# Performance work log

Hardware: AMD Instinct MI355X
Metric: run time of the kernel (lower is better)

The kernel has to match this reference:

```python
import jax, jax.numpy as jnp
import numpy as np
import math

INPUT_SIZE = 512
DK = 64
B, N = 8, 2048

def setup_inputs() -> dict:
    key = jax.random.key(0)
    k1, k2, k3, k4, k5, k6 = jax.random.split(key, 6)
    X = jax.random.normal(k1, (B, N, INPUT_SIZE), dtype=jnp.float32)
    h = jax.random.normal(k2, (B, N, INPUT_SIZE), dtype=jnp.float32)
    s = 1.0 / math.sqrt(INPUT_SIZE)
    WQ = jax.random.uniform(k3, (INPUT_SIZE, DK), dtype=jnp.float32, minval=-s, maxval=s)
    bQ = jax.random.uniform(k4, (DK,), dtype=jnp.float32, minval=-s, maxval=s)
    WK = jax.random.uniform(k5, (INPUT_SIZE, DK), dtype=jnp.float32, minval=-s, maxval=s)
    bK = jax.random.uniform(k6, (DK,), dtype=jnp.float32, minval=-s, maxval=s)
    return {"X": X, "h": h, "WQ": WQ, "bQ": bQ, "WK": WK, "bK": bK}

def reference(X, h, WQ, bQ, WK, bK):
    # Q = linearQ(h), K = linearK(X); dropout is eval-mode identity
    Q = jnp.einsum('bnd,dk->bnk', h, WQ) + bQ   # [B, N, dk]
    K = jnp.einsum('bnd,dk->bnk', X, WK) + bK   # [B, N, dk]
    scores = jnp.einsum('bqk,bnk->bqn', Q, K) / jnp.sqrt(jnp.asarray(DK, X.dtype))
    A = jax.nn.softmax(scores, axis=-1)          # [B, N, N]
    out = jnp.einsum('bqn,bnd->bqd', A, X)       # V = X
    return out
```

## Files before the change

### kernel.cpp

```cpp
#include <hip/hip_runtime.h>
#include <hip/hip_bf16.h>

#define B_ 8
#define N_ 2048
#define D_ 512
#define DK_ 64

typedef float f32x4 __attribute__((ext_vector_type(4)));
typedef short bf16x8 __attribute__((ext_vector_type(8)));
typedef unsigned short u16;

__device__ __forceinline__ u16 f2bf(float f) {
  union { float f; unsigned u; } v; v.f = f;
  unsigned r = v.u + 0x7FFFu + ((v.u >> 16) & 1u);
  return (u16)(r >> 16);
}

#define MFMA32(a, b, cacc) __builtin_amdgcn_mfma_f32_16x16x32_bf16((a), (b), (cacc), 0, 0, 0)

#define BARRIER_LGKM() do {                                   \
    asm volatile("s_waitcnt lgkmcnt(0)" ::: "memory");        \
    __builtin_amdgcn_s_barrier();                             \
    asm volatile("" ::: "memory");                            \
  } while (0)


__global__ __launch_bounds__(256) void prep_kernel(
    const float* __restrict__ h, const float* __restrict__ X,
    const float* __restrict__ WQ, const float* __restrict__ bQ,
    const float* __restrict__ WK, const float* __restrict__ bK,
    u16* __restrict__ Qf, u16* __restrict__ Kf, u16* __restrict__ Vf) {
  int bid = blockIdx.x;
  int b = bid & 7, nt = bid >> 3;
  int n0 = nt * 64;
  int t = threadIdx.x, w = t >> 6, l = t & 63, g = l >> 4, c = l & 15;

  __shared__ u16 Xb16[64][520];

  int arow = n0 + w * 16 + c;
  const float* hrow = h + ((size_t)b * N_ + arow) * D_;
  const float* Xrow = X + ((size_t)b * N_ + arow) * D_;
  f32x4 accq[4], acck[4];
#pragma unroll
  for (int cf = 0; cf < 4; ++cf) {
    accq[cf] = (f32x4){0.f, 0.f, 0.f, 0.f};
    acck[cf] = (f32x4){0.f, 0.f, 0.f, 0.f};
  }
  for (int k0 = 0; k0 < D_; k0 += 32) {
    bf16x8 ah, ax;
    {
      f32x4 h0 = *reinterpret_cast<const f32x4*>(hrow + k0 + 8 * g);
      f32x4 h1 = *reinterpret_cast<const f32x4*>(hrow + k0 + 8 * g + 4);
      f32x4 x0 = *reinterpret_cast<const f32x4*>(Xrow + k0 + 8 * g);
      f32x4 x1 = *reinterpret_cast<const f32x4*>(Xrow + k0 + 8 * g + 4);
#pragma unroll
      for (int i = 0; i < 4; ++i) {
        ah[i] = (short)f2bf(h0[i]); ah[i + 4] = (short)f2bf(h1[i]);
        ax[i] = (short)f2bf(x0[i]); ax[i + 4] = (short)f2bf(x1[i]);
      }
    }
    *reinterpret_cast<bf16x8*>(&Xb16[w * 16 + c][k0 + 8 * g]) = ax;
#pragma unroll
    for (int cf = 0; cf < 4; ++cf) {
      bf16x8 bq, bk;
#pragma unroll
      for (int i = 0; i < 8; ++i) {
        int kk = k0 + 8 * g + i;
        bq[i] = (short)f2bf(WQ[(size_t)kk * DK_ + cf * 16 + c]);
        bk[i] = (short)f2bf(WK[(size_t)kk * DK_ + cf * 16 + c]);
      }
      accq[cf] = MFMA32(ah, bq, accq[cf]);
      acck[cf] = MFMA32(ax, bk, acck[cf]);
    }
  }
#pragma unroll
  for (int cf = 0; cf < 4; ++cf) {
    float vq = bQ[cf * 16 + c], vk = bK[cf * 16 + c];
    int ks = cf >> 1;
    int g2 = ((cf & 1) * 16 + c) >> 3;
    int i2 = c & 7;
#pragma unroll
    for (int r = 0; r < 4; ++r) {
      size_t e = ((size_t)(b * 128 + nt * 4 + w) * 2 + ks) * 512 +
                 (g2 * 16 + 4 * g + r) * 8 + i2;
      Qf[e] = f2bf((accq[cf][r] + vq) * 0.125f);
      Kf[e] = f2bf(acck[cf][r] + vk);
    }
  }

  __syncthreads();

#pragma unroll
  for (int dtl = 0; dtl < 8; ++dtl) {
    int dt = w * 8 + dtl;
#pragma unroll
    for (int ks = 0; ks < 2; ++ks) {
      bf16x8 v;
#pragma unroll
      for (int i = 0; i < 8; ++i) v[i] = Xb16[ks * 32 + 8 * g + i][dt * 16 + c];
      *reinterpret_cast<bf16x8*>(
          Vf + (((size_t)(b * 32 + dt) * 32 + nt) * 2 + ks) * 512 + l * 8) = v;
    }
  }
}

__global__ __launch_bounds__(512, 1) void attn_kernel(
    const u16* __restrict__ Qf, const u16* __restrict__ Kf,
    const u16* __restrict__ Vf, float* __restrict__ out) {
  int bid = blockIdx.x;
  int b = bid & 7, qt = bid >> 3;
  int q0 = qt * 64;
  int t = threadIdx.x, w = t >> 6, l = t & 63, g = l >> 4, c = l & 15;
  int qh = w >> 1, kq = w & 1;

  __shared__ u16 Plds[4][64][40];
  __shared__ float Lp[2][64];

  bf16x8 aq[2];
#pragma unroll
  for (int ks = 0; ks < 2; ++ks)
    aq[ks] = *reinterpret_cast<const bf16x8*>(
        Qf + ((size_t)(b * 128 + qt * 4 + qh) * 2 + ks) * 512 + l * 8);

  f32x4 o[4][4];
#pragma unroll
  for (int a = 0; a < 4; ++a)
#pragma unroll
    for (int d = 0; d < 4; ++d) o[a][d] = (f32x4){0.f, 0.f, 0.f, 0.f};
  float lp[4] = {0.f, 0.f, 0.f, 0.f};

  const u16* Kbase = Kf + ((size_t)(b * 256 + 2 * kq)) * 512 + l * 8;
  const u16* Vbase = Vf + ((size_t)(b * 32 + w * 4) * 64) * 512 + l * 8;

  bf16x8 kbuf[4][2], vbuf[4][4];

#pragma unroll
  for (int j = 0; j < 4; ++j) {
#pragma unroll
    for (int ks = 0; ks < 2; ++ks)
      kbuf[j][ks] = *reinterpret_cast<const bf16x8*>(
          Kbase + (size_t)(4 * j + ks) * 512);
#pragma unroll
    for (int f = 0; f < 4; ++f)
      vbuf[j][f] = *reinterpret_cast<const bf16x8*>(
          Vbase + (size_t)(f * 64 + j) * 512);
  }
#pragma unroll
  for (int j0 = 0; j0 < 2; ++j0) {
    f32x4 s = (f32x4){0.f, 0.f, 0.f, 0.f};
    s = MFMA32(aq[0], kbuf[j0][0], s);
    s = MFMA32(aq[1], kbuf[j0][1], s);
#pragma unroll
    for (int r = 0; r < 4; ++r) {
      float p = __expf(s[r]); lp[r] += p;
      Plds[j0][qh * 16 + 4 * g + r][kq * 16 + c] = f2bf(p);
    }
  }
  BARRIER_LGKM();

  auto pair = [&](bf16x8 (&kS0)[2], bf16x8 (&kS1)[2],
                  bf16x8 (&kL0)[2], bf16x8 (&kL1)[2],
                  bf16x8 (&vR0)[4], bf16x8 (&vR1)[4],
                  int k2, int pW0, int pW1, int pR0, int pR1) {
    const int jA = (k2 + 4) & 63, jB = (k2 + 5) & 63;

#pragma unroll
    for (int ks = 0; ks < 2; ++ks)
      kL0[ks] = *reinterpret_cast<const bf16x8*>(
          Kbase + (size_t)(4 * jA + ks) * 512);
#pragma unroll
    for (int ks = 0; ks < 2; ++ks)
      kL1[ks] = *reinterpret_cast<const bf16x8*>(
          Kbase + (size_t)(4 * jB + ks) * 512);

    {
      f32x4 s = (f32x4){0.f, 0.f, 0.f, 0.f};
      s = MFMA32(aq[0], kS0[0], s);
      s = MFMA32(aq[1], kS0[1], s);
#pragma unroll
      for (int r = 0; r < 4; ++r) {
        float p = __expf(s[r]); lp[r] += p;
        Plds[pW0][qh * 16 + 4 * g + r][kq * 16 + c] = f2bf(p);
      }
    }
    {
      f32x4 s = (f32x4){0.f, 0.f, 0.f, 0.f};
      s = MFMA32(aq[0], kS1[0], s);
      s = MFMA32(aq[1], kS1[1], s);
#pragma unroll
      for (int r = 0; r < 4; ++r) {
        float p = __expf(s[r]); lp[r] += p;
        Plds[pW1][qh * 16 + 4 * g + r][kq * 16 + c] = f2bf(p);
      }
    }

    {
      bf16x8 pa0 = *reinterpret_cast<const bf16x8*>(&Plds[pR0][c][8 * g]);
      bf16x8 pa1 = *reinterpret_cast<const bf16x8*>(&Plds[pR0][16 + c][8 * g]);
      bf16x8 pa2 = *reinterpret_cast<const bf16x8*>(&Plds[pR0][32 + c][8 * g]);
      bf16x8 pa3 = *reinterpret_cast<const bf16x8*>(&Plds[pR0][48 + c][8 * g]);
      __builtin_amdgcn_s_setprio(1);
#pragma unroll
      for (int dt = 0; dt < 4; ++dt) {
        o[0][dt] = MFMA32(pa0, vR0[dt], o[0][dt]);
        o[1][dt] = MFMA32(pa1, vR0[dt], o[1][dt]);
        o[2][dt] = MFMA32(pa2, vR0[dt], o[2][dt]);
        o[3][dt] = MFMA32(pa3, vR0[dt], o[3][dt]);
      }
      __builtin_amdgcn_s_setprio(0);
    }
#pragma unroll
    for (int f = 0; f < 4; ++f)
      vR0[f] = *reinterpret_cast<const bf16x8*>(
          Vbase + (size_t)(f * 64 + jA) * 512);

    {
      bf16x8 pa0 = *reinterpret_cast<const bf16x8*>(&Plds[pR1][c][8 * g]);
      bf16x8 pa1 = *reinterpret_cast<const bf16x8*>(&Plds[pR1][16 + c][8 * g]);
      bf16x8 pa2 = *reinterpret_cast<const bf16x8*>(&Plds[pR1][32 + c][8 * g]);
      bf16x8 pa3 = *reinterpret_cast<const bf16x8*>(&Plds[pR1][48 + c][8 * g]);
      __builtin_amdgcn_s_setprio(1);
#pragma unroll
      for (int dt = 0; dt < 4; ++dt) {
        o[0][dt] = MFMA32(pa0, vR1[dt], o[0][dt]);
        o[1][dt] = MFMA32(pa1, vR1[dt], o[1][dt]);
        o[2][dt] = MFMA32(pa2, vR1[dt], o[2][dt]);
        o[3][dt] = MFMA32(pa3, vR1[dt], o[3][dt]);
      }
      __builtin_amdgcn_s_setprio(0);
    }
#pragma unroll
    for (int f = 0; f < 4; ++f)
      vR1[f] = *reinterpret_cast<const bf16x8*>(
          Vbase + (size_t)(f * 64 + jB) * 512);

    BARRIER_LGKM();
  };

#pragma unroll 1
  for (int k2 = 0; k2 < 60; k2 += 4) {
    pair(kbuf[2], kbuf[3], kbuf[0], kbuf[1], vbuf[0], vbuf[1], k2,     2, 3, 0, 1);
    pair(kbuf[0], kbuf[1], kbuf[2], kbuf[3], vbuf[2], vbuf[3], k2 + 2, 0, 1, 2, 3);
  }
  pair(kbuf[2], kbuf[3], kbuf[0], kbuf[1], vbuf[0], vbuf[1], 60, 2, 3, 0, 1);

#pragma unroll
  for (int e = 0; e < 2; ++e) {
    const int pb = 2 + e;
    bf16x8 pa0 = *reinterpret_cast<const bf16x8*>(&Plds[pb][c][8 * g]);
    bf16x8 pa1 = *reinterpret_cast<const bf16x8*>(&Plds[pb][16 + c][8 * g]);
    bf16x8 pa2 = *reinterpret_cast<const bf16x8*>(&Plds[pb][32 + c][8 * g]);
    bf16x8 pa3 = *reinterpret_cast<const bf16x8*>(&Plds[pb][48 + c][8 * g]);
#pragma unroll
    for (int dt = 0; dt < 4; ++dt) {
      o[0][dt] = MFMA32(pa0, vbuf[pb][dt], o[0][dt]);
      o[1][dt] = MFMA32(pa1, vbuf[pb][dt], o[1][dt]);
      o[2][dt] = MFMA32(pa2, vbuf[pb][dt], o[2][dt]);
      o[3][dt] = MFMA32(pa3, vbuf[pb][dt], o[3][dt]);
    }
  }

#pragma unroll
  for (int r = 0; r < 4; ++r) {
    float v = lp[r];
    v += __shfl_xor(v, 1); v += __shfl_xor(v, 2);
    v += __shfl_xor(v, 4); v += __shfl_xor(v, 8);
    lp[r] = v;
  }
  if (c == 0) {
#pragma unroll
    for (int r = 0; r < 4; ++r) Lp[kq][qh * 16 + 4 * g + r] = lp[r];
  }
  __syncthreads();

  float* outb = out + ((size_t)b * N_ + q0) * D_;
#pragma unroll
  for (int qf2 = 0; qf2 < 4; ++qf2)
#pragma unroll
    for (int r = 0; r < 4; ++r) {
      int ql = qf2 * 16 + 4 * g + r;
      float L = Lp[0][ql] + Lp[1][ql];
      float inv = 1.0f / L;
#pragma unroll
      for (int df = 0; df < 4; ++df)
        outb[(size_t)ql * D_ + w * 64 + df * 16 + c] = o[qf2][df][r] * inv;
    }
}

extern "C" void kernel_launch(void* const* d_in, const int* in_sizes, int n_in,
                              void* d_out, int out_size, void* d_ws, size_t ws_size,
                              hipStream_t stream) {
  const float* X  = (const float*)d_in[0];
  const float* h  = (const float*)d_in[1];
  const float* WQ = (const float*)d_in[2];
  const float* bQ = (const float*)d_in[3];
  const float* WK = (const float*)d_in[4];
  const float* bK = (const float*)d_in[5];
  float* out = (float*)d_out;

  u16* Vf = (u16*)d_ws;
  u16* Qf = Vf + (size_t)B_ * D_ * N_;
  u16* Kf = Qf + (size_t)B_ * N_ * DK_;

  prep_kernel<<<dim3(256), dim3(256), 0, stream>>>(h, X, WQ, bQ, WK, bK, Qf, Kf, Vf);
  attn_kernel<<<dim3(256), dim3(512), 0, stream>>>(Qf, Kf, Vf, out);
}
```

Before: 73.36 us.

## Double attention block to 16 waves, split D across waves with producer subset

Attention blocks now launch 1024 threads (16 waves). The first 8 waves act as producers that compute QK^T scores and exponentials into LDS, and all 16 waves consume P to compute PV, each covering 32 output columns instead of 64. The K/V register prefetch depth is cut to one pair, and score computation is reordered to happen after the PV MFMAs within each step. The intent is more latency hiding and fewer registers per wave, at the cost of idle producer slots in half the waves and a shallower prefetch pipeline.

```diff
diff --git a/kernel.cpp b/kernel.cpp
--- a/kernel.cpp
+++ b/kernel.cpp
@@ -104,93 +104,81 @@
   }
 }
 
-__global__ __launch_bounds__(512, 1) void attn_kernel(
+__global__ __launch_bounds__(1024, 4) void attn_kernel(
     const u16* __restrict__ Qf, const u16* __restrict__ Kf,
     const u16* __restrict__ Vf, float* __restrict__ out) {
   int bid = blockIdx.x;
   int b = bid & 7, qt = bid >> 3;
   int q0 = qt * 64;
   int t = threadIdx.x, w = t >> 6, l = t & 63, g = l >> 4, c = l & 15;
-  int qh = w >> 1, kq = w & 1;
+  int qh = (w >> 1) & 3, kq = w & 1;
+  const bool prod = (w < 8);
 
   __shared__ u16 Plds[4][64][40];
   __shared__ float Lp[2][64];
 
   bf16x8 aq[2];
-#pragma unroll
-  for (int ks = 0; ks < 2; ++ks)
-    aq[ks] = *reinterpret_cast<const bf16x8*>(
-        Qf + ((size_t)(b * 128 + qt * 4 + qh) * 2 + ks) * 512 + l * 8);
-
-  f32x4 o[4][4];
+  if (prod) {
+#pragma unroll
+    for (int ks = 0; ks < 2; ++ks)
+      aq[ks] = *reinterpret_cast<const bf16x8*>(
+          Qf + ((size_t)(b * 128 + qt * 4 + qh) * 2 + ks) * 512 + l * 8);
+  }
+
+  f32x4 o[4][2];
 #pragma unroll
   for (int a = 0; a < 4; ++a)
 #pragma unroll
-    for (int d = 0; d < 4; ++d) o[a][d] = (f32x4){0.f, 0.f, 0.f, 0.f};
+    for (int f = 0; f < 2; ++f) o[a][f] = (f32x4){0.f, 0.f, 0.f, 0.f};
   float lp[4] = {0.f, 0.f, 0.f, 0.f};
 
   const u16* Kbase = Kf + ((size_t)(b * 256 + 2 * kq)) * 512 + l * 8;
-  const u16* Vbase = Vf + ((size_t)(b * 32 + w * 4) * 64) * 512 + l * 8;
-
-  bf16x8 kbuf[4][2], vbuf[4][4];
-
-#pragma unroll
-  for (int j = 0; j < 4; ++j) {
-#pragma unroll
-    for (int ks = 0; ks < 2; ++ks)
-      kbuf[j][ks] = *reinterpret_cast<const bf16x8*>(
-          Kbase + (size_t)(4 * j + ks) * 512);
-#pragma unroll
-    for (int f = 0; f < 4; ++f)
-      vbuf[j][f] = *reinterpret_cast<const bf16x8*>(
-          Vbase + (size_t)(f * 64 + j) * 512);
-  }
-#pragma unroll
-  for (int j0 = 0; j0 < 2; ++j0) {
-    f32x4 s = (f32x4){0.f, 0.f, 0.f, 0.f};
-    s = MFMA32(aq[0], kbuf[j0][0], s);
-    s = MFMA32(aq[1], kbuf[j0][1], s);
-#pragma unroll
-    for (int r = 0; r < 4; ++r) {
-      float p = __expf(s[r]); lp[r] += p;
-      Plds[j0][qh * 16 + 4 * g + r][kq * 16 + c] = f2bf(p);
-    }
-  }
-  BARRIER_LGKM();
-
-  auto pair = [&](bf16x8 (&kS0)[2], bf16x8 (&kS1)[2],
-                  bf16x8 (&kL0)[2], bf16x8 (&kL1)[2],
-                  bf16x8 (&vR0)[4], bf16x8 (&vR1)[4],
-                  int k2, int pW0, int pW1, int pR0, int pR1) {
-    const int jA = (k2 + 4) & 63, jB = (k2 + 5) & 63;
-
-#pragma unroll
-    for (int ks = 0; ks < 2; ++ks)
-      kL0[ks] = *reinterpret_cast<const bf16x8*>(
-          Kbase + (size_t)(4 * jA + ks) * 512);
-#pragma unroll
-    for (int ks = 0; ks < 2; ++ks)
-      kL1[ks] = *reinterpret_cast<const bf16x8*>(
-          Kbase + (size_t)(4 * jB + ks) * 512);
-
+  const u16* Vbase = Vf + ((size_t)(b * 32 + w * 2) * 64) * 512 + l * 8;
+
+  bf16x8 kb0[2], kb1[2], vb0[2], vb1[2];
+
+  if (prod) {
+#pragma unroll
+    for (int ks = 0; ks < 2; ++ks) {
+      kb0[ks] = *reinterpret_cast<const bf16x8*>(Kbase + (size_t)ks * 512);
+      kb1[ks] = *reinterpret_cast<const bf16x8*>(Kbase + (size_t)(4 + ks) * 512);
+    }
+  }
+#pragma unroll
+  for (int f = 0; f < 2; ++f) {
+    vb0[f] = *reinterpret_cast<const bf16x8*>(Vbase + (size_t)(f * 64 + 0) * 512);
+    vb1[f] = *reinterpret_cast<const bf16x8*>(Vbase + (size_t)(f * 64 + 1) * 512);
+  }
+  if (prod) {
     {
       f32x4 s = (f32x4){0.f, 0.f, 0.f, 0.f};
-      s = MFMA32(aq[0], kS0[0], s);
-      s = MFMA32(aq[1], kS0[1], s);
+      s = MFMA32(aq[0], kb0[0], s); s = MFMA32(aq[1], kb0[1], s);
 #pragma unroll
       for (int r = 0; r < 4; ++r) {
         float p = __expf(s[r]); lp[r] += p;
-        Plds[pW0][qh * 16 + 4 * g + r][kq * 16 + c] = f2bf(p);
+        Plds[0][qh * 16 + 4 * g + r][kq * 16 + c] = f2bf(p);
       }
     }
     {
       f32x4 s = (f32x4){0.f, 0.f, 0.f, 0.f};
-      s = MFMA32(aq[0], kS1[0], s);
-      s = MFMA32(aq[1], kS1[1], s);
+      s = MFMA32(aq[0], kb1[0], s); s = MFMA32(aq[1], kb1[1], s);
 #pragma unroll
       for (int r = 0; r < 4; ++r) {
         float p = __expf(s[r]); lp[r] += p;
-        Plds[pW1][qh * 16 + 4 * g + r][kq * 16 + c] = f2bf(p);
+        Plds[1][qh * 16 + 4 * g + r][kq * 16 + c] = f2bf(p);
+      }
+    }
+  }
+  BARRIER_LGKM();
+
+  auto pair = [&](int k2, int pR0, int pR1, int pW0, int pW1) {
+    if (prod) {
+#pragma unroll
+      for (int ks = 0; ks < 2; ++ks) {
+        kb0[ks] = *reinterpret_cast<const bf16x8*>(
+            Kbase + (size_t)(4 * (k2 + 2) + ks) * 512);
+        kb1[ks] = *reinterpret_cast<const bf16x8*>(
+            Kbase + (size_t)(4 * (k2 + 3) + ks) * 512);
       }
     }
 
@@ -201,18 +189,18 @@
       bf16x8 pa3 = *reinterpret_cast<const bf16x8*>(&Plds[pR0][48 + c][8 * g]);
       __builtin_amdgcn_s_setprio(1);
 #pragma unroll
-      for (int dt = 0; dt < 4; ++dt) {
-        o[0][dt] = MFMA32(pa0, vR0[dt], o[0][dt]);
-        o[1][dt] = MFMA32(pa1, vR0[dt], o[1][dt]);
-        o[2][dt] = MFMA32(pa2, vR0[dt], o[2][dt]);
-        o[3][dt] = MFMA32(pa3, vR0[dt], o[3][dt]);
+      for (int f = 0; f < 2; ++f) {
+        o[0][f] = MFMA32(pa0, vb0[f], o[0][f]);
+        o[1][f] = MFMA32(pa1, vb0[f], o[1][f]);
+        o[2][f] = MFMA32(pa2, vb0[f], o[2][f]);
+        o[3][f] = MFMA32(pa3, vb0[f], o[3][f]);
       }
       __builtin_amdgcn_s_setprio(0);
     }
 #pragma unroll
-    for (int f = 0; f < 4; ++f)
-      vR0[f] = *reinterpret_cast<const bf16x8*>(
-          Vbase + (size_t)(f * 64 + jA) * 512);
+    for (int f = 0; f < 2; ++f)
+      vb0[f] = *reinterpret_cast<const bf16x8*>(
+          Vbase + (size_t)(f * 64 + k2 + 2) * 512);
 
     {
       bf16x8 pa0 = *reinterpret_cast<const bf16x8*>(&Plds[pR1][c][8 * g]);
@@ -221,28 +209,49 @@
       bf16x8 pa3 = *reinterpret_cast<const bf16x8*>(&Plds[pR1][48 + c][8 * g]);
       __builtin_amdgcn_s_setprio(1);
 #pragma unroll
-      for (int dt = 0; dt < 4; ++dt) {
-        o[0][dt] = MFMA32(pa0, vR1[dt], o[0][dt]);
-        o[1][dt] = MFMA32(pa1, vR1[dt], o[1][dt]);
-        o[2][dt] = MFMA32(pa2, vR1[dt], o[2][dt]);
-        o[3][dt] = MFMA32(pa3, vR1[dt], o[3][dt]);
+      for (int f = 0; f < 2; ++f) {
+        o[0][f] = MFMA32(pa0, vb1[f], o[0][f]);
+        o[1][f] = MFMA32(pa1, vb1[f], o[1][f]);
+        o[2][f] = MFMA32(pa2, vb1[f], o[2][f]);
+        o[3][f] = MFMA32(pa3, vb1[f], o[3][f]);
       }
       __builtin_amdgcn_s_setprio(0);
     }
 #pragma unroll
-    for (int f = 0; f < 4; ++f)
-      vR1[f] = *reinterpret_cast<const bf16x8*>(
-          Vbase + (size_t)(f * 64 + jB) * 512);
+    for (int f = 0; f < 2; ++f)
+      vb1[f] = *reinterpret_cast<const bf16x8*>(
+          Vbase + (size_t)(f * 64 + k2 + 3) * 512);
+
+    if (prod) {
+      {
+        f32x4 s = (f32x4){0.f, 0.f, 0.f, 0.f};
+        s = MFMA32(aq[0], kb0[0], s); s = MFMA32(aq[1], kb0[1], s);
+#pragma unroll
+        for (int r = 0; r < 4; ++r) {
+          float p = __expf(s[r]); lp[r] += p;
+          Plds[pW0][qh * 16 + 4 * g + r][kq * 16 + c] = f2bf(p);
+        }
+      }
+      {
+        f32x4 s = (f32x4){0.f, 0.f, 0.f, 0.f};
+        s = MFMA32(aq[0], kb1[0], s); s = MFMA32(aq[1], kb1[1], s);
+#pragma unroll
+        for (int r = 0; r < 4; ++r) {
+          float p = __expf(s[r]); lp[r] += p;
+          Plds[pW1][qh * 16 + 4 * g + r][kq * 16 + c] = f2bf(p);
+        }
+      }
+    }
 
     BARRIER_LGKM();
   };
 
 #pragma unroll 1
   for (int k2 = 0; k2 < 60; k2 += 4) {
-    pair(kbuf[2], kbuf[3], kbuf[0], kbuf[1], vbuf[0], vbuf[1], k2,     2, 3, 0, 1);
-    pair(kbuf[0], kbuf[1], kbuf[2], kbuf[3], vbuf[2], vbuf[3], k2 + 2, 0, 1, 2, 3);
-  }
-  pair(kbuf[2], kbuf[3], kbuf[0], kbuf[1], vbuf[0], vbuf[1], 60, 2, 3, 0, 1);
+    pair(k2, 0, 1, 2, 3);
+    pair(k2 + 2, 2, 3, 0, 1);
+  }
+  pair(60, 0, 1, 2, 3);
 
 #pragma unroll
   for (int e = 0; e < 2; ++e) {
@@ -252,38 +261,41 @@
     bf16x8 pa2 = *reinterpret_cast<const bf16x8*>(&Plds[pb][32 + c][8 * g]);
     bf16x8 pa3 = *reinterpret_cast<const bf16x8*>(&Plds[pb][48 + c][8 * g]);
 #pragma unroll
-    for (int dt = 0; dt < 4; ++dt) {
-      o[0][dt] = MFMA32(pa0, vbuf[pb][dt], o[0][dt]);
-      o[1][dt] = MFMA32(pa1, vbuf[pb][dt], o[1][dt]);
-      o[2][dt] = MFMA32(pa2, vbuf[pb][dt], o[2][dt]);
-      o[3][dt] = MFMA32(pa3, vbuf[pb][dt], o[3][dt]);
-    }
-  }
-
-#pragma unroll
-  for (int r = 0; r < 4; ++r) {
-    float v = lp[r];
-    v += __shfl_xor(v, 1); v += __shfl_xor(v, 2);
-    v += __shfl_xor(v, 4); v += __shfl_xor(v, 8);
-    lp[r] = v;
-  }
-  if (c == 0) {
-#pragma unroll
-    for (int r = 0; r < 4; ++r) Lp[kq][qh * 16 + 4 * g + r] = lp[r];
+    for (int f = 0; f < 2; ++f) {
+      bf16x8 vv = e ? vb1[f] : vb0[f];
+      o[0][f] = MFMA32(pa0, vv, o[0][f]);
+      o[1][f] = MFMA32(pa1, vv, o[1][f]);
+      o[2][f] = MFMA32(pa2, vv, o[2][f]);
+      o[3][f] = MFMA32(pa3, vv, o[3][f]);
+    }
+  }
+
+  if (prod) {
+#pragma unroll
+    for (int r = 0; r < 4; ++r) {
+      float v = lp[r];
+      v += __shfl_xor(v, 1); v += __shfl_xor(v, 2);
+      v += __shfl_xor(v, 4); v += __shfl_xor(v, 8);
+      lp[r] = v;
+    }
+    if (c == 0) {
+#pragma unroll
+      for (int r = 0; r < 4; ++r) Lp[kq][qh * 16 + 4 * g + r] = lp[r];
+    }
   }
   __syncthreads();
 
   float* outb = out + ((size_t)b * N_ + q0) * D_;
 #pragma unroll
-  for (int qf2 = 0; qf2 < 4; ++qf2)
+  for (int a = 0; a < 4; ++a)
 #pragma unroll
     for (int r = 0; r < 4; ++r) {
-      int ql = qf2 * 16 + 4 * g + r;
+      int ql = a * 16 + 4 * g + r;
       float L = Lp[0][ql] + Lp[1][ql];
       float inv = 1.0f / L;
 #pragma unroll
-      for (int df = 0; df < 4; ++df)
-        outb[(size_t)ql * D_ + w * 64 + df * 16 + c] = o[qf2][df][r] * inv;
+      for (int f = 0; f < 2; ++f)
+        outb[(size_t)ql * D_ + w * 32 + f * 16 + c] = o[a][f][r] * inv;
     }
 }
 
@@ -303,5 +315,5 @@
   u16* Kf = Qf + (size_t)B_ * N_ * DK_;
 
   prep_kernel<<<dim3(256), dim3(256), 0, stream>>>(h, X, WQ, bQ, WK, bK, Qf, Kf, Vf);
-  attn_kernel<<<dim3(256), dim3(512), 0, stream>>>(Qf, Kf, Vf, out);
+  attn_kernel<<<dim3(256), dim3(1024), 0, stream>>>(Qf, Kf, Vf, out);
 }
```

Result: no change. 74.71 us (+1.8%).
